# Kernel optimization log

Hardware: AMD Instinct MI355X
Metric: run time of the kernel (lower is better)

Reference implementation:

```python
import jax, jax.numpy as jnp
import numpy as np

D_MODEL = 64
TEMPER = float(np.power(D_MODEL, 0.5))  # d_model ** temper_value


def setup_inputs() -> dict:
    key = jax.random.key(0)
    k1, k2, k3, k4 = jax.random.split(key, 4)
    BH, L, D = 16, 2048, 64  # batch*heads, seq_len, head_dim
    return {
        "q": jax.random.normal(k1, (BH, L, D), dtype=jnp.float32),
        "k": jax.random.normal(k2, (BH, L, D), dtype=jnp.float32),
        "v": jax.random.normal(k3, (BH, L, D), dtype=jnp.float32),
        "position_dpa": jax.random.normal(k4, (BH, L, D), dtype=jnp.float32),
    }


def reference(q, k, v, position_dpa):
    # attn = q @ k^T / temper               -> [BH, L, L]
    attn = jnp.einsum("bqd,bkd->bqk", q, k) / TEMPER
    # attn_pos = q @ position_dpa^T / temper -> [BH, L, L]
    attn_pos = jnp.einsum("bqd,bkd->bqk", q, position_dpa) / TEMPER
    # positional mixing bmm: attn @ attn_pos -> [BH, L, L]
    attn = jnp.einsum("bqk,bkp->bqp", attn, attn_pos)
    attn = jax.nn.softmax(attn, axis=-1)  # dropout p=0 -> identity
    out = jnp.einsum("bqk,bkd->bqd", attn, v)
    return out, attn
```

## Files before the change

kernel.cpp:

```cpp
#include <hip/hip_runtime.h>
#include <cstdint>

#define BH  16
#define SEQ 2048
#define DIM 64
#define OUT_ELEMS (BH*SEQ*DIM)

typedef float f32x4 __attribute__((ext_vector_type(4)));
typedef float f32x2 __attribute__((ext_vector_type(2)));
typedef short bf16x8 __attribute__((ext_vector_type(8)));
typedef unsigned short u16;
typedef unsigned short u16x4 __attribute__((ext_vector_type(4)));

#define MFMA16 __builtin_amdgcn_mfma_f32_16x16x32_bf16

#define SROW      2052
#define VTM_OFF   (16*SROW)
#define TL_OFF    (VTM_OFF + 4352)
#define QS_OFF    (TL_OFF + 1024)
#define RED_OFF   (QS_OFF + 1024)
#define LDS_FLOATS (RED_OFF + 160)
#define LDS_BYTES  (LDS_FLOATS*4)

__device__ __forceinline__ u16 f2bf(float x){
  uint32_t u = __float_as_uint(x);
  return (u16)((u + 0x7fffu + ((u>>16)&1u)) >> 16);
}
__device__ __forceinline__ void split8(f32x4 a, f32x4 b, bf16x8& hi, bf16x8& lo){
  float v[8] = {a.x,a.y,a.z,a.w,b.x,b.y,b.z,b.w};
  #pragma unroll
  for (int i=0;i<8;i++){
    uint32_t u  = __float_as_uint(v[i]);
    uint32_t hb = u & 0xffff0000u;
    hi[i] = (short)(hb>>16);
    lo[i] = (short)f2bf(v[i] - __uint_as_float(hb));
  }
}
__device__ __forceinline__ bf16x8 pack8(f32x4 a, f32x4 b){
  bf16x8 r;
  r[0]=(short)f2bf(a.x); r[1]=(short)f2bf(a.y); r[2]=(short)f2bf(a.z); r[3]=(short)f2bf(a.w);
  r[4]=(short)f2bf(b.x); r[5]=(short)f2bf(b.y); r[6]=(short)f2bf(b.z); r[7]=(short)f2bf(b.w);
  return r;
}

__global__ __launch_bounds__(256) void kA1(const float* __restrict__ kk,
                                           const float* __restrict__ qq,
                                           float* __restrict__ part){
  __shared__ __align__(16) float kl[64][68];
  __shared__ __align__(16) float ql[64][68];
  const int b   = blockIdx.y;
  const int ch  = blockIdx.x;
  const int tid = threadIdx.x;
  const int j     = tid & 63;
  const int ibase = (tid >> 6) * 16;
  const int lrow  = tid >> 2;
  const int lcol  = (tid & 3) * 16;
  const float* kb = kk + (size_t)b*SEQ*DIM;
  const float* qb = qq + (size_t)b*SEQ*DIM;
  float acc[16];
  #pragma unroll
  for (int i=0;i<16;i++) acc[i]=0.f;
  for (int sub=0; sub<2; ++sub){
    const int l0 = ch*128 + sub*64;
    const f32x4* ks = (const f32x4*)(kb + (size_t)(l0+lrow)*DIM + lcol);
    const f32x4* qs = (const f32x4*)(qb + (size_t)(l0+lrow)*DIM + lcol);
    f32x4 kv[4], qv[4];
    #pragma unroll
    for (int i=0;i<4;i++){ kv[i]=ks[i]; qv[i]=qs[i]; }
    __syncthreads();
    #pragma unroll
    for (int i=0;i<4;i++){
      *(f32x4*)&kl[lrow][lcol+4*i] = kv[i];
      *(f32x4*)&ql[lrow][lcol+4*i] = qv[i];
    }
    __syncthreads();
    for (int t=0; t<64; ++t){
      const float qv1 = ql[t][j];
      const f32x4 k0 = *(const f32x4*)&kl[t][ibase];
      const f32x4 k1 = *(const f32x4*)&kl[t][ibase+4];
      const f32x4 k2 = *(const f32x4*)&kl[t][ibase+8];
      const f32x4 k3 = *(const f32x4*)&kl[t][ibase+12];
      acc[0]+=k0.x*qv1; acc[1]+=k0.y*qv1; acc[2]+=k0.z*qv1; acc[3]+=k0.w*qv1;
      acc[4]+=k1.x*qv1; acc[5]+=k1.y*qv1; acc[6]+=k1.z*qv1; acc[7]+=k1.w*qv1;
      acc[8]+=k2.x*qv1; acc[9]+=k2.y*qv1; acc[10]+=k2.z*qv1; acc[11]+=k2.w*qv1;
      acc[12]+=k3.x*qv1; acc[13]+=k3.y*qv1; acc[14]+=k3.z*qv1; acc[15]+=k3.w*qv1;
    }
  }
  float* pp = part + (size_t)(b*16+ch)*4096;
  #pragma unroll
  for (int ii=0; ii<16; ++ii)
    pp[(ibase+ii)*64 + j] = acc[ii];
}

__global__ __launch_bounds__(256) void kA2(const float* __restrict__ part,
                                           float* __restrict__ M){
  const int idx = blockIdx.x*256 + threadIdx.x;
  const int b = idx >> 12, o = idx & 4095;
  float s = 0.f;
  #pragma unroll
  for (int ch=0; ch<16; ++ch)
    s += part[(size_t)(b*16+ch)*4096 + o];
  M[(size_t)b*4096 + o] = s * (1.0f/64.0f);
}

__global__ __launch_bounds__(512,2) void kB(const float* __restrict__ q,
                                            const float* __restrict__ pos,
                                            const float* __restrict__ v,
                                            const float* __restrict__ M,
                                            float* __restrict__ outp,
                                            float* __restrict__ attn){
  extern __shared__ __align__(16) float smem[];
  float* S    = smem;
  float* VTM  = smem + VTM_OFF;
  u16*   vT   = (u16*)VTM;
  float* Tl   = smem + TL_OFF;
  float* qs   = smem + QS_OFF;
  float* red  = smem + RED_OFF;
  float* mrow = red + 128;
  float* linv = mrow + 16;

  const int blk   = blockIdx.x;
  const int xcd   = blk & 7;
  const int slot  = blk >> 3;
  const int b     = xcd*2 + (slot & 1);
  const int bslot = slot >> 1;
  const int tid   = threadIdx.x;
  const int lane  = tid & 63;
  const int w     = tid >> 6;
  const int quad  = lane >> 4;
  const int l16   = lane & 15;

  const float* pb = pos + (size_t)b*SEQ*DIM;
  const float* vb = v   + (size_t)b*SEQ*DIM;
  const float* qb = q   + (size_t)b*SEQ*DIM;
  const float* Mb = M   + (size_t)b*4096;

  for (int t = 0; t < 8; ++t){
    const int r0 = (bslot*8 + t) * 16;
    __syncthreads();

    {
      const f32x4* Mg = (const f32x4*)Mb;
      f32x4* Md = (f32x4*)VTM;
      Md[tid]     = Mg[tid];
      Md[tid+512] = Mg[tid+512];
      if (tid < 256)
        ((f32x4*)qs)[tid] = ((const f32x4*)(qb + (size_t)r0*DIM))[tid];
    }
    __syncthreads();

    {
      const int r = tid >> 5;
      const int e = tid & 31;
      float a0 = 0.f, a1 = 0.f;
      #pragma unroll 8
      for (int d=0; d<64; ++d){
        const float qd = qs[r*64 + d];
        a0 += qd * VTM[d*64 + e];
        a1 += qd * VTM[d*64 + e + 32];
      }
      Tl[r*64 + e]      = a0;
      Tl[r*64 + e + 32] = a1;
    }
    __syncthreads();

    bf16x8 Ah[2], Al[2];
    #pragma unroll
    for (int h=0; h<2; ++h){
      const float* ts = &Tl[l16*64 + h*32 + quad*8];
      split8(*(const f32x4*)ts, *(const f32x4*)(ts+4), Ah[h], Al[h]);
    }

    #pragma unroll 2
    for (int tt=0; tt<16; ++tt){
      const int c0 = w*256 + tt*16;
      const float* pr = pb + (size_t)(c0 + l16)*DIM + quad*8;
      f32x4 p0 = *(const f32x4*)pr;
      f32x4 p1 = *(const f32x4*)(pr+4);
      f32x4 p2 = *(const f32x4*)(pr+32);
      f32x4 p3 = *(const f32x4*)(pr+36);
      bf16x8 Bh0, Bl0, Bh1, Bl1;
      split8(p0, p1, Bh0, Bl0);
      split8(p2, p3, Bh1, Bl1);
      f32x4 acc = {0.f,0.f,0.f,0.f};
      acc = MFMA16(Ah[0], Bh0, acc, 0,0,0);
      acc = MFMA16(Al[0], Bh0, acc, 0,0,0);
      acc = MFMA16(Ah[0], Bl0, acc, 0,0,0);
      acc = MFMA16(Ah[1], Bh1, acc, 0,0,0);
      acc = MFMA16(Al[1], Bh1, acc, 0,0,0);
      acc = MFMA16(Ah[1], Bl1, acc, 0,0,0);
      #pragma unroll
      for (int i=0;i<4;i++)
        S[(quad*4+i)*SROW + c0 + l16] = acc[i];
    }
    __syncthreads();

    {
      const int r = tid & 15, seg = tid >> 4;
      const f32x4* sr = (const f32x4*)&S[r*SROW + seg*64];
      float m = -3.0e38f;
      #pragma unroll
      for (int i=0;i<16;i++){
        const f32x4 x = sr[i];
        m = fmaxf(m, fmaxf(fmaxf(x.x,x.y), fmaxf(x.z,x.w)));
      }
      m = fmaxf(m, __shfl_xor(m, 16, 64));
      m = fmaxf(m, __shfl_xor(m, 32, 64));
      if (lane < 16) red[w*16 + lane] = m;
    }
    __syncthreads();
    if (tid < 16){
      float m = red[tid];
      #pragma unroll
      for (int w2=1; w2<8; ++w2) m = fmaxf(m, red[w2*16 + tid]);
      mrow[tid] = m;
    }
    __syncthreads();

    {
      const int r = tid & 15, seg = tid >> 4;
      const float mr = mrow[r];
      f32x4* sr = (f32x4*)&S[r*SROW + seg*64];
      float s = 0.f;
      #pragma unroll
      for (int i=0;i<16;i++){
        f32x4 x = sr[i];
        x.x = __expf(x.x - mr); x.y = __expf(x.y - mr);
        x.z = __expf(x.z - mr); x.w = __expf(x.w - mr);
        sr[i] = x;
        s += x.x + x.y + x.z + x.w;
      }
      s += __shfl_xor(s, 16, 64);
      s += __shfl_xor(s, 32, 64);
      if (lane < 16) red[w*16 + lane] = s;
    }
    __syncthreads();
    if (tid < 16){
      float s = red[tid];
      #pragma unroll
      for (int w2=1; w2<8; ++w2) s += red[w2*16 + tid];
      linv[tid] = 1.0f / s;
    }
    __syncthreads();

    {
      const int r  = tid >> 5;
      const int cq = (tid & 31) * 4;
      const float li = linv[r];
      float* ab = attn + ((size_t)b*SEQ + r0 + r)*(size_t)SEQ;
      const float* sr = &S[r*SROW];
      #pragma unroll
      for (int j=0;j<16;++j){
        const int c = cq + 128*j;
        f32x4 val = *(const f32x4*)(sr + c);
        val.x *= li; val.y *= li; val.z *= li; val.w *= li;
        __builtin_nontemporal_store(val, (f32x4*)(ab + c));
      }
    }

    f32x4 pacc0 = {0.f,0.f,0.f,0.f}, pacc1 = {0.f,0.f,0.f,0.f};
    const int kch   = w >> 1;
    const int npair = w & 1;
    for (int vt=0; vt<16; ++vt){
      __syncthreads();
      {
        const int c4 = (tid & 31)*4;
        const int d4 = (tid >> 5)*4;
        const int cg = vt*128 + c4;
        f32x4 r0v = *(const f32x4*)(vb + (size_t)(cg  )*DIM + d4);
        f32x4 r1v = *(const f32x4*)(vb + (size_t)(cg+1)*DIM + d4);
        f32x4 r2v = *(const f32x4*)(vb + (size_t)(cg+2)*DIM + d4);
        f32x4 r3v = *(const f32x4*)(vb + (size_t)(cg+3)*DIM + d4);
        const float rr[4][4] = {{r0v.x,r1v.x,r2v.x,r3v.x},
                                {r0v.y,r1v.y,r2v.y,r3v.y},
                                {r0v.z,r1v.z,r2v.z,r3v.z},
                                {r0v.w,r1v.w,r2v.w,r3v.w}};
        #pragma unroll
        for (int dd=0; dd<4; ++dd){
          u16x4 pk;
          pk[0]=f2bf(rr[dd][0]); pk[1]=f2bf(rr[dd][1]);
          pk[2]=f2bf(rr[dd][2]); pk[3]=f2bf(rr[dd][3]);
          *(u16x4*)&vT[(d4+dd)*136 + c4] = pk;
        }
      }
      __syncthreads();
      {
        const int cbase = kch*32;
        const float* es = &S[l16*SROW + vt*128 + cbase + quad*8];
        const bf16x8 Af = pack8(*(const f32x4*)es, *(const f32x4*)(es+4));
        const int n0 = (npair*2)*16 + l16;
        const int n1 = n0 + 16;
        const bf16x8 B0 = *(const bf16x8*)&vT[n0*136 + cbase + quad*8];
        const bf16x8 B1 = *(const bf16x8*)&vT[n1*136 + cbase + quad*8];
        pacc0 = MFMA16(Af, B0, pacc0, 0,0,0);
        pacc1 = MFMA16(Af, B1, pacc1, 0,0,0);
      }
    }
    __syncthreads();
    {
      float* Pf = S;
      #pragma unroll
      for (int i=0;i<4;i++){
        Pf[(w*2+0)*256 + (quad*4+i)*16 + l16] = pacc0[i];
        Pf[(w*2+1)*256 + (quad*4+i)*16 + l16] = pacc1[i];
      }
      pacc0 = (f32x4){0.f,0.f,0.f,0.f};
      pacc1 = (f32x4){0.f,0.f,0.f,0.f};
    }
    __syncthreads();
    {
      const int o = tid*2;
      const int m = o >> 6;
      const int d = o & 63;
      const int nt = d >> 4;
      float s0 = 0.f, s1 = 0.f;
      #pragma unroll
      for (int kk=0; kk<4; ++kk){
        const int sl = (2*kk + (nt>>1))*2 + (nt&1);
        s0 += S[sl*256 + m*16 + (d&15)];
        s1 += S[sl*256 + m*16 + (d&15) + 1];
      }
      const float li = linv[m];
      f32x2 res; res.x = s0*li; res.y = s1*li;
      *(f32x2*)(outp + ((size_t)b*SEQ + r0 + m)*DIM + d) = res;
    }
  }
}

extern "C" void kernel_launch(void* const* d_in, const int* in_sizes, int n_in,
                              void* d_out, int out_size, void* d_ws, size_t ws_size,
                              hipStream_t stream){
  const float* q = (const float*)d_in[0];
  const float* k = (const float*)d_in[1];
  const float* v = (const float*)d_in[2];
  const float* p = (const float*)d_in[3];
  float* out  = (float*)d_out;
  float* attn = out + OUT_ELEMS;
  float* M    = (float*)d_ws;
  float* part = attn;

  static int lds_set = 0;
  (void)lds_set;
  hipFuncSetAttribute((const void*)kB,
                      hipFuncAttributeMaxDynamicSharedMemorySize, LDS_BYTES);

  kA1<<<dim3(16,16), 256, 0, stream>>>(k, q, part);
  kA2<<<dim3(256),   256, 0, stream>>>(part, M);
  kB <<<dim3(256),   512, LDS_BYTES, stream>>>(q, p, v, M, out, attn);
}
```

Baseline: 613.1 us.

## Keep score tile in registers, store bf16 probabilities, double-buffer V, atomic-reduce M

The mixed attention row tile now stays in MFMA accumulator registers through the max, exp and sum steps, and is written once to LDS as bf16 for the P·V product. This removes the fp32 LDS round trips and the repeated per-element conversion. The P·V loop now uses 256-column chunks with double-buffered, register-prefetched V transposes, and the position tile loads are software-prefetched. The K^T·Q reduction replaces the partial-sum kernel with atomicAdd after a memset. Register pressure rises and occupancy drops to one block per CU, and the atomic summation order is nondeterministic.

```diff
diff --git a/kernel.cpp b/kernel.cpp
--- a/kernel.cpp
+++ b/kernel.cpp
@@ -10,17 +10,16 @@
 typedef float f32x2 __attribute__((ext_vector_type(2)));
 typedef short bf16x8 __attribute__((ext_vector_type(8)));
 typedef unsigned short u16;
-typedef unsigned short u16x4 __attribute__((ext_vector_type(4)));
+typedef unsigned short u16x8 __attribute__((ext_vector_type(8)));
 
 #define MFMA16 __builtin_amdgcn_mfma_f32_16x16x32_bf16
 
-#define SROW      2052
-#define VTM_OFF   (16*SROW)
-#define TL_OFF    (VTM_OFF + 4352)
-#define QS_OFF    (TL_OFF + 1024)
-#define RED_OFF   (QS_OFF + 1024)
-#define LDS_FLOATS (RED_OFF + 160)
-#define LDS_BYTES  (LDS_FLOATS*4)
+#define S2_RS     2056
+#define S2_BYTES  (16*S2_RS*2)
+#define VT_RS     264
+#define VT_HALVES (64*VT_RS)
+#define VT_BYTES  (2*VT_HALVES*2)
+#define LDS_BYTES (S2_BYTES + VT_BYTES + 640)
 
 __device__ __forceinline__ u16 f2bf(float x){
   uint32_t u = __float_as_uint(x);
@@ -36,16 +35,10 @@
     lo[i] = (short)f2bf(v[i] - __uint_as_float(hb));
   }
 }
-__device__ __forceinline__ bf16x8 pack8(f32x4 a, f32x4 b){
-  bf16x8 r;
-  r[0]=(short)f2bf(a.x); r[1]=(short)f2bf(a.y); r[2]=(short)f2bf(a.z); r[3]=(short)f2bf(a.w);
-  r[4]=(short)f2bf(b.x); r[5]=(short)f2bf(b.y); r[6]=(short)f2bf(b.z); r[7]=(short)f2bf(b.w);
-  return r;
-}
-
-__global__ __launch_bounds__(256) void kA1(const float* __restrict__ kk,
-                                           const float* __restrict__ qq,
-                                           float* __restrict__ part){
+
+__global__ __launch_bounds__(256) void kA(const float* __restrict__ kk,
+                                          const float* __restrict__ qq,
+                                          float* __restrict__ M){
   __shared__ __align__(16) float kl[64][68];
   __shared__ __align__(16) float ql[64][68];
   const int b   = blockIdx.y;
@@ -55,69 +48,53 @@
   const int ibase = (tid >> 6) * 16;
   const int lrow  = tid >> 2;
   const int lcol  = (tid & 3) * 16;
-  const float* kb = kk + (size_t)b*SEQ*DIM;
-  const float* qb = qq + (size_t)b*SEQ*DIM;
+  const int l0    = ch * 64;
+  const f32x4* ks = (const f32x4*)(kk + ((size_t)b*SEQ + l0 + lrow)*DIM + lcol);
+  const f32x4* qs = (const f32x4*)(qq + ((size_t)b*SEQ + l0 + lrow)*DIM + lcol);
+  f32x4 kv[4], qv[4];
+  #pragma unroll
+  for (int i=0;i<4;i++){ kv[i]=ks[i]; qv[i]=qs[i]; }
+  #pragma unroll
+  for (int i=0;i<4;i++){
+    *(f32x4*)&kl[lrow][lcol+4*i] = kv[i];
+    *(f32x4*)&ql[lrow][lcol+4*i] = qv[i];
+  }
+  __syncthreads();
   float acc[16];
   #pragma unroll
   for (int i=0;i<16;i++) acc[i]=0.f;
-  for (int sub=0; sub<2; ++sub){
-    const int l0 = ch*128 + sub*64;
-    const f32x4* ks = (const f32x4*)(kb + (size_t)(l0+lrow)*DIM + lcol);
-    const f32x4* qs = (const f32x4*)(qb + (size_t)(l0+lrow)*DIM + lcol);
-    f32x4 kv[4], qv[4];
-    #pragma unroll
-    for (int i=0;i<4;i++){ kv[i]=ks[i]; qv[i]=qs[i]; }
-    __syncthreads();
-    #pragma unroll
-    for (int i=0;i<4;i++){
-      *(f32x4*)&kl[lrow][lcol+4*i] = kv[i];
-      *(f32x4*)&ql[lrow][lcol+4*i] = qv[i];
-    }
-    __syncthreads();
-    for (int t=0; t<64; ++t){
-      const float qv1 = ql[t][j];
-      const f32x4 k0 = *(const f32x4*)&kl[t][ibase];
-      const f32x4 k1 = *(const f32x4*)&kl[t][ibase+4];
-      const f32x4 k2 = *(const f32x4*)&kl[t][ibase+8];
-      const f32x4 k3 = *(const f32x4*)&kl[t][ibase+12];
-      acc[0]+=k0.x*qv1; acc[1]+=k0.y*qv1; acc[2]+=k0.z*qv1; acc[3]+=k0.w*qv1;
-      acc[4]+=k1.x*qv1; acc[5]+=k1.y*qv1; acc[6]+=k1.z*qv1; acc[7]+=k1.w*qv1;
-      acc[8]+=k2.x*qv1; acc[9]+=k2.y*qv1; acc[10]+=k2.z*qv1; acc[11]+=k2.w*qv1;
-      acc[12]+=k3.x*qv1; acc[13]+=k3.y*qv1; acc[14]+=k3.z*qv1; acc[15]+=k3.w*qv1;
-    }
+  for (int t=0; t<64; ++t){
+    const float qv1 = ql[t][j];
+    const f32x4 k0 = *(const f32x4*)&kl[t][ibase];
+    const f32x4 k1 = *(const f32x4*)&kl[t][ibase+4];
+    const f32x4 k2 = *(const f32x4*)&kl[t][ibase+8];
+    const f32x4 k3 = *(const f32x4*)&kl[t][ibase+12];
+    acc[0]+=k0.x*qv1; acc[1]+=k0.y*qv1; acc[2]+=k0.z*qv1; acc[3]+=k0.w*qv1;
+    acc[4]+=k1.x*qv1; acc[5]+=k1.y*qv1; acc[6]+=k1.z*qv1; acc[7]+=k1.w*qv1;
+    acc[8]+=k2.x*qv1; acc[9]+=k2.y*qv1; acc[10]+=k2.z*qv1; acc[11]+=k2.w*qv1;
+    acc[12]+=k3.x*qv1; acc[13]+=k3.y*qv1; acc[14]+=k3.z*qv1; acc[15]+=k3.w*qv1;
   }
-  float* pp = part + (size_t)(b*16+ch)*4096;
+  float* mp = M + (size_t)b*4096;
   #pragma unroll
   for (int ii=0; ii<16; ++ii)
-    pp[(ibase+ii)*64 + j] = acc[ii];
-}
-
-__global__ __launch_bounds__(256) void kA2(const float* __restrict__ part,
-                                           float* __restrict__ M){
-  const int idx = blockIdx.x*256 + threadIdx.x;
-  const int b = idx >> 12, o = idx & 4095;
-  float s = 0.f;
-  #pragma unroll
-  for (int ch=0; ch<16; ++ch)
-    s += part[(size_t)(b*16+ch)*4096 + o];
-  M[(size_t)b*4096 + o] = s * (1.0f/64.0f);
-}
-
-__global__ __launch_bounds__(512,2) void kB(const float* __restrict__ q,
+    atomicAdd(&mp[(ibase+ii)*64 + j], acc[ii] * (1.0f/64.0f));
+}
+
+__global__ __launch_bounds__(512,1) void kB(const float* __restrict__ q,
                                             const float* __restrict__ pos,
                                             const float* __restrict__ v,
                                             const float* __restrict__ M,
                                             float* __restrict__ outp,
                                             float* __restrict__ attn){
-  extern __shared__ __align__(16) float smem[];
-  float* S    = smem;
-  float* VTM  = smem + VTM_OFF;
-  u16*   vT   = (u16*)VTM;
-  float* Tl   = smem + TL_OFF;
-  float* qs   = smem + QS_OFF;
-  float* red  = smem + RED_OFF;
+  extern __shared__ __align__(16) char smem[];
+  u16*   S2   = (u16*)smem;
+  u16*   vT   = (u16*)(smem + S2_BYTES);
+  float* Uf   = (float*)(smem + S2_BYTES);
+  float* red  = (float*)(smem + S2_BYTES + VT_BYTES);
   float* mrow = red + 128;
   float* linv = mrow + 16;
+  float* qs   = Uf + 4096;
+  float* Tl   = Uf + 5120;
 
   const int blk   = blockIdx.x;
   const int xcd   = blk & 7;
@@ -141,14 +118,13 @@
 
     {
       const f32x4* Mg = (const f32x4*)Mb;
-      f32x4* Md = (f32x4*)VTM;
+      f32x4* Md = (f32x4*)Uf;
       Md[tid]     = Mg[tid];
       Md[tid+512] = Mg[tid+512];
       if (tid < 256)
         ((f32x4*)qs)[tid] = ((const f32x4*)(qb + (size_t)r0*DIM))[tid];
     }
     __syncthreads();
-
     {
       const int r = tid >> 5;
       const int e = tid & 31;
@@ -156,8 +132,8 @@
       #pragma unroll 8
       for (int d=0; d<64; ++d){
         const float qd = qs[r*64 + d];
-        a0 += qd * VTM[d*64 + e];
-        a1 += qd * VTM[d*64 + e + 32];
+        a0 += qd * Uf[d*64 + e];
+        a1 += qd * Uf[d*64 + e + 32];
       }
       Tl[r*64 + e]      = a0;
       Tl[r*64 + e + 32] = a1;
@@ -167,46 +143,57 @@
     bf16x8 Ah[2], Al[2];
     #pragma unroll
     for (int h=0; h<2; ++h){
-      const float* ts = &Tl[l16*64 + h*32 + quad*8];
+      const float* ts = Tl + l16*64 + h*32 + quad*8;
       split8(*(const f32x4*)ts, *(const f32x4*)(ts+4), Ah[h], Al[h]);
     }
 
-    #pragma unroll 2
-    for (int tt=0; tt<16; ++tt){
-      const int c0 = w*256 + tt*16;
-      const float* pr = pb + (size_t)(c0 + l16)*DIM + quad*8;
+    f32x4 Sreg[16];
+    {
+      const float* pr = pb + (size_t)(w*256 + l16)*DIM + quad*8;
       f32x4 p0 = *(const f32x4*)pr;
       f32x4 p1 = *(const f32x4*)(pr+4);
       f32x4 p2 = *(const f32x4*)(pr+32);
       f32x4 p3 = *(const f32x4*)(pr+36);
-      bf16x8 Bh0, Bl0, Bh1, Bl1;
-      split8(p0, p1, Bh0, Bl0);
-      split8(p2, p3, Bh1, Bl1);
-      f32x4 acc = {0.f,0.f,0.f,0.f};
-      acc = MFMA16(Ah[0], Bh0, acc, 0,0,0);
-      acc = MFMA16(Al[0], Bh0, acc, 0,0,0);
-      acc = MFMA16(Ah[0], Bl0, acc, 0,0,0);
-      acc = MFMA16(Ah[1], Bh1, acc, 0,0,0);
-      acc = MFMA16(Al[1], Bh1, acc, 0,0,0);
-      acc = MFMA16(Ah[1], Bl1, acc, 0,0,0);
-      #pragma unroll
-      for (int i=0;i<4;i++)
-        S[(quad*4+i)*SROW + c0 + l16] = acc[i];
-    }
-    __syncthreads();
-
-    {
-      const int r = tid & 15, seg = tid >> 4;
-      const f32x4* sr = (const f32x4*)&S[r*SROW + seg*64];
-      float m = -3.0e38f;
-      #pragma unroll
-      for (int i=0;i<16;i++){
-        const f32x4 x = sr[i];
-        m = fmaxf(m, fmaxf(fmaxf(x.x,x.y), fmaxf(x.z,x.w)));
-      }
-      m = fmaxf(m, __shfl_xor(m, 16, 64));
-      m = fmaxf(m, __shfl_xor(m, 32, 64));
-      if (lane < 16) red[w*16 + lane] = m;
+      #pragma unroll
+      for (int tt=0; tt<16; ++tt){
+        f32x4 n0,n1,n2,n3;
+        if (tt < 15){
+          const float* pn = pb + (size_t)(w*256 + (tt+1)*16 + l16)*DIM + quad*8;
+          n0 = *(const f32x4*)pn;
+          n1 = *(const f32x4*)(pn+4);
+          n2 = *(const f32x4*)(pn+32);
+          n3 = *(const f32x4*)(pn+36);
+        }
+        bf16x8 Bh0, Bl0, Bh1, Bl1;
+        split8(p0, p1, Bh0, Bl0);
+        split8(p2, p3, Bh1, Bl1);
+        f32x4 acc = {0.f,0.f,0.f,0.f};
+        acc = MFMA16(Ah[0], Bh0, acc, 0,0,0);
+        acc = MFMA16(Al[0], Bh0, acc, 0,0,0);
+        acc = MFMA16(Ah[0], Bl0, acc, 0,0,0);
+        acc = MFMA16(Ah[1], Bh1, acc, 0,0,0);
+        acc = MFMA16(Al[1], Bh1, acc, 0,0,0);
+        acc = MFMA16(Ah[1], Bl1, acc, 0,0,0);
+        Sreg[tt] = acc;
+        p0=n0; p1=n1; p2=n2; p3=n3;
+      }
+    }
+
+    float mloc[4];
+    #pragma unroll
+    for (int i=0;i<4;i++) mloc[i] = -3.0e38f;
+    #pragma unroll
+    for (int tt=0; tt<16; ++tt)
+      #pragma unroll
+      for (int i=0;i<4;i++) mloc[i] = fmaxf(mloc[i], Sreg[tt][i]);
+    #pragma unroll
+    for (int i=0;i<4;i++){
+      float m = mloc[i];
+      m = fmaxf(m, __shfl_xor(m, 1, 64));
+      m = fmaxf(m, __shfl_xor(m, 2, 64));
+      m = fmaxf(m, __shfl_xor(m, 4, 64));
+      m = fmaxf(m, __shfl_xor(m, 8, 64));
+      if (l16 == 0) red[w*16 + quad*4 + i] = m;
     }
     __syncthreads();
     if (tid < 16){
@@ -217,22 +204,25 @@
     }
     __syncthreads();
 
-    {
-      const int r = tid & 15, seg = tid >> 4;
-      const float mr = mrow[r];
-      f32x4* sr = (f32x4*)&S[r*SROW + seg*64];
-      float s = 0.f;
-      #pragma unroll
-      for (int i=0;i<16;i++){
-        f32x4 x = sr[i];
-        x.x = __expf(x.x - mr); x.y = __expf(x.y - mr);
-        x.z = __expf(x.z - mr); x.w = __expf(x.w - mr);
-        sr[i] = x;
-        s += x.x + x.y + x.z + x.w;
-      }
-      s += __shfl_xor(s, 16, 64);
-      s += __shfl_xor(s, 32, 64);
-      if (lane < 16) red[w*16 + lane] = s;
+    float mr[4], sloc[4];
+    #pragma unroll
+    for (int i=0;i<4;i++){ mr[i] = mrow[quad*4+i]; sloc[i] = 0.f; }
+    #pragma unroll
+    for (int tt=0; tt<16; ++tt)
+      #pragma unroll
+      for (int i=0;i<4;i++){
+        const float e = __expf(Sreg[tt][i] - mr[i]);
+        Sreg[tt][i] = e;
+        sloc[i] += e;
+      }
+    #pragma unroll
+    for (int i=0;i<4;i++){
+      float s = sloc[i];
+      s += __shfl_xor(s, 1, 64);
+      s += __shfl_xor(s, 2, 64);
+      s += __shfl_xor(s, 4, 64);
+      s += __shfl_xor(s, 8, 64);
+      if (l16 == 0) red[w*16 + quad*4 + i] = s;
     }
     __syncthreads();
     if (tid < 16){
@@ -244,82 +234,77 @@
     __syncthreads();
 
     {
-      const int r  = tid >> 5;
-      const int cq = (tid & 31) * 4;
-      const float li = linv[r];
-      float* ab = attn + ((size_t)b*SEQ + r0 + r)*(size_t)SEQ;
-      const float* sr = &S[r*SROW];
-      #pragma unroll
-      for (int j=0;j<16;++j){
-        const int c = cq + 128*j;
-        f32x4 val = *(const f32x4*)(sr + c);
-        val.x *= li; val.y *= li; val.z *= li; val.w *= li;
-        __builtin_nontemporal_store(val, (f32x4*)(ab + c));
-      }
-    }
-
-    f32x4 pacc0 = {0.f,0.f,0.f,0.f}, pacc1 = {0.f,0.f,0.f,0.f};
-    const int kch   = w >> 1;
-    const int npair = w & 1;
-    for (int vt=0; vt<16; ++vt){
+      float li[4];
+      #pragma unroll
+      for (int i=0;i<4;i++) li[i] = linv[quad*4+i];
+      float* ab = attn + ((size_t)b*SEQ + r0)*(size_t)SEQ;
+      #pragma unroll
+      for (int tt=0; tt<16; ++tt){
+        const int c = w*256 + tt*16 + l16;
+        #pragma unroll
+        for (int i=0;i<4;i++){
+          const int row = quad*4+i;
+          __builtin_nontemporal_store(Sreg[tt][i]*li[i],
+                                      ab + (size_t)row*SEQ + c);
+          S2[row*S2_RS + c] = f2bf(Sreg[tt][i]);
+        }
+      }
+    }
+    __syncthreads();
+
+    const int khalf = w >> 2;
+    const int ntile = w & 3;
+    const int c8 = (tid & 31) * 8;
+    const int d4 = (tid >> 5) * 4;
+    f32x4 pacc = {0.f,0.f,0.f,0.f};
+    f32x4 cur[8];
+    #pragma unroll
+    for (int cc=0; cc<8; ++cc)
+      cur[cc] = *(const f32x4*)(vb + (size_t)(c8+cc)*DIM + d4);
+    #pragma unroll 1
+    for (int r=0; r<8; ++r){
+      f32x4 nxt[8];
+      if (r < 7){
+        #pragma unroll
+        for (int cc=0; cc<8; ++cc)
+          nxt[cc] = *(const f32x4*)(vb + (size_t)((r+1)*256 + c8 + cc)*DIM + d4);
+      }
+      u16* dst = vT + (r&1)*VT_HALVES;
+      #pragma unroll
+      for (int dd=0; dd<4; ++dd){
+        u16x8 pk;
+        #pragma unroll
+        for (int cc=0; cc<8; ++cc) pk[cc] = f2bf(cur[cc][dd]);
+        *(u16x8*)&dst[(d4+dd)*VT_RS + c8] = pk;
+      }
       __syncthreads();
-      {
-        const int c4 = (tid & 31)*4;
-        const int d4 = (tid >> 5)*4;
-        const int cg = vt*128 + c4;
-        f32x4 r0v = *(const f32x4*)(vb + (size_t)(cg  )*DIM + d4);
-        f32x4 r1v = *(const f32x4*)(vb + (size_t)(cg+1)*DIM + d4);
-        f32x4 r2v = *(const f32x4*)(vb + (size_t)(cg+2)*DIM + d4);
-        f32x4 r3v = *(const f32x4*)(vb + (size_t)(cg+3)*DIM + d4);
-        const float rr[4][4] = {{r0v.x,r1v.x,r2v.x,r3v.x},
-                                {r0v.y,r1v.y,r2v.y,r3v.y},
-                                {r0v.z,r1v.z,r2v.z,r3v.z},
-                                {r0v.w,r1v.w,r2v.w,r3v.w}};
-        #pragma unroll
-        for (int dd=0; dd<4; ++dd){
-          u16x4 pk;
-          pk[0]=f2bf(rr[dd][0]); pk[1]=f2bf(rr[dd][1]);
-          pk[2]=f2bf(rr[dd][2]); pk[3]=f2bf(rr[dd][3]);
-          *(u16x4*)&vT[(d4+dd)*136 + c4] = pk;
-        }
-      }
-      __syncthreads();
-      {
-        const int cbase = kch*32;
-        const float* es = &S[l16*SROW + vt*128 + cbase + quad*8];
-        const bf16x8 Af = pack8(*(const f32x4*)es, *(const f32x4*)(es+4));
-        const int n0 = (npair*2)*16 + l16;
-        const int n1 = n0 + 16;
-        const bf16x8 B0 = *(const bf16x8*)&vT[n0*136 + cbase + quad*8];
-        const bf16x8 B1 = *(const bf16x8*)&vT[n1*136 + cbase + quad*8];
-        pacc0 = MFMA16(Af, B0, pacc0, 0,0,0);
-        pacc1 = MFMA16(Af, B1, pacc1, 0,0,0);
-      }
-    }
-    __syncthreads();
-    {
-      float* Pf = S;
-      #pragma unroll
-      for (int i=0;i<4;i++){
-        Pf[(w*2+0)*256 + (quad*4+i)*16 + l16] = pacc0[i];
-        Pf[(w*2+1)*256 + (quad*4+i)*16 + l16] = pacc1[i];
-      }
-      pacc0 = (f32x4){0.f,0.f,0.f,0.f};
-      pacc1 = (f32x4){0.f,0.f,0.f,0.f};
+      const u16* vbuf = vT + (r&1)*VT_HALVES;
+      #pragma unroll
+      for (int kk=0; kk<4; ++kk){
+        const int cb = khalf*128 + kk*32;
+        const bf16x8 Af = *(const bf16x8*)&S2[l16*S2_RS + r*256 + cb + quad*8];
+        const bf16x8 Bf = *(const bf16x8*)&vbuf[(ntile*16 + l16)*VT_RS + cb + quad*8];
+        pacc = MFMA16(Af, Bf, pacc, 0,0,0);
+      }
+      #pragma unroll
+      for (int cc=0; cc<8; ++cc) cur[cc] = nxt[cc];
+    }
+    __syncthreads();
+    {
+      float* Pout = (float*)vT;
+      #pragma unroll
+      for (int i=0;i<4;i++)
+        Pout[w*256 + (quad*4+i)*16 + l16] = pacc[i];
     }
     __syncthreads();
     {
       const int o = tid*2;
       const int m = o >> 6;
       const int d = o & 63;
-      const int nt = d >> 4;
-      float s0 = 0.f, s1 = 0.f;
-      #pragma unroll
-      for (int kk=0; kk<4; ++kk){
-        const int sl = (2*kk + (nt>>1))*2 + (nt&1);
-        s0 += S[sl*256 + m*16 + (d&15)];
-        s1 += S[sl*256 + m*16 + (d&15) + 1];
-      }
+      const float* Pout = (const float*)vT;
+      const int w_a = d >> 4, col = d & 15;
+      float s0 = Pout[w_a*256 + m*16 + col]     + Pout[(w_a+4)*256 + m*16 + col];
+      float s1 = Pout[w_a*256 + m*16 + col + 1] + Pout[(w_a+4)*256 + m*16 + col + 1];
       const float li = linv[m];
       f32x2 res; res.x = s0*li; res.y = s1*li;
       *(f32x2*)(outp + ((size_t)b*SEQ + r0 + m)*DIM + d) = res;
@@ -337,14 +322,11 @@
   float* out  = (float*)d_out;
   float* attn = out + OUT_ELEMS;
   float* M    = (float*)d_ws;
-  float* part = attn;
-
-  static int lds_set = 0;
-  (void)lds_set;
+
   hipFuncSetAttribute((const void*)kB,
                       hipFuncAttributeMaxDynamicSharedMemorySize, LDS_BYTES);
 
-  kA1<<<dim3(16,16), 256, 0, stream>>>(k, q, part);
-  kA2<<<dim3(256),   256, 0, stream>>>(part, M);
-  kB <<<dim3(256),   512, LDS_BYTES, stream>>>(q, p, v, M, out, attn);
-}
+  hipMemsetAsync(d_ws, 0, BH*4096*sizeof(float), stream);
+  kA<<<dim3(32,16), 256, 0, stream>>>(k, q, M);
+  kB<<<dim3(256),   512, LDS_BYTES, stream>>>(q, p, v, M, out, attn);
+}
```

Result: slower. 653.4 us (+6.6%).
